# Kernel tuning notes

Measured on AMD Instinct MI355X. Metric: run time of the kernel, lower is better.

## Reference

```python
import jax, jax.numpy as jnp
import numpy as np

B, N, DIN, HID = 64, 1024, 128, 128
NEG = 9000000000000000.0


def setup_inputs() -> dict:
    key = jax.random.key(0)
    ks = jax.random.split(key, 8)
    s = 1.0 / np.sqrt(DIN)
    x = jax.random.normal(ks[0], (B, N, DIN), dtype=jnp.float32)
    mask = jax.random.randint(ks[1], (B, N, N), 0, 2, dtype=jnp.int32)
    Wv = jax.random.uniform(ks[2], (HID, DIN), jnp.float32, -s, s)
    bv = jax.random.uniform(ks[3], (HID,), jnp.float32, -s, s)
    Wk = jax.random.uniform(ks[4], (HID, DIN), jnp.float32, -s, s)
    bk = jax.random.uniform(ks[5], (HID,), jnp.float32, -s, s)
    Wq = jax.random.uniform(ks[6], (HID, DIN), jnp.float32, -s, s)
    bq = jax.random.uniform(ks[7], (HID,), jnp.float32, -s, s)
    return {"x": x, "mask": mask, "Wv": Wv, "bv": bv, "Wk": Wk, "bk": bk, "Wq": Wq, "bq": bq}


def reference(x, mask, Wv, bv, Wk, bk, Wq, bq):
    m = mask.astype(x.dtype)                       # [B,N,N]
    v = jnp.tanh(jnp.einsum('bnd,hd->bnh', x, Wv) + bv)  # [B,N,H]
    q = jnp.tanh(jnp.einsum('bnd,hd->bnh', x, Wq) + bq)
    k = jnp.tanh(jnp.einsum('bnd,hd->bnh', x, Wk) + bk)
    scores = jnp.einsum('bih,bjh->bij', q, k)      # bmm(q, k^T)
    att = jax.nn.softmax(scores * m - NEG * (1.0 - m), axis=2)
    out = jnp.einsum('bij,bjh->bih', att, v)       # [B,N,H]
    return out
```

## Files before the change

### kernel.cpp

```cpp
#include <hip/hip_runtime.h>
#include <cstdint>
#include <cstddef>

#define BB 64
#define NN 1024
#define DD 128

typedef short    bf16x8 __attribute__((ext_vector_type(8)));
typedef _Float16 f16x8  __attribute__((ext_vector_type(8)));
typedef float    f32x4  __attribute__((ext_vector_type(4)));

__device__ __forceinline__ unsigned short f2bf(float f) {
  union { float f; unsigned u; } v; v.f = f;
  unsigned r = v.u + 0x7FFFu + ((v.u >> 16) & 1u);
  return (unsigned short)(r >> 16);
}
__device__ __forceinline__ unsigned short f2h(float f) {
  union { _Float16 h; unsigned short u; } v; v.h = (_Float16)f;
  return v.u;
}
__device__ __forceinline__ float fast_tanh(float x) {
  x = fminf(15.0f, fmaxf(-15.0f, x));
  float e = __expf(2.0f * x);
  return (e - 1.0f) / (e + 1.0f);
}

__device__ __forceinline__ void async_copy16(void* lptr, const void* gptr) {
  __builtin_amdgcn_global_load_lds(
      (const __attribute__((address_space(1))) unsigned int*)gptr,
      (__attribute__((address_space(3))) unsigned int*)lptr, 16, 0, 0);
}

__global__ __launch_bounds__(256, 2) void proj_kernel(
    const float* __restrict__ x,
    const float* __restrict__ Wq, const float* __restrict__ bq,
    const float* __restrict__ Wk, const float* __restrict__ bk,
    const float* __restrict__ Wv, const float* __restrict__ bv,
    unsigned short* __restrict__ qg,
    unsigned short* __restrict__ kg,
    unsigned short* __restrict__ vtg)
{
  __shared__ unsigned short wlds[128 * 136];

  const int tid  = threadIdx.x;
  const int lane = tid & 63;
  const int wave = tid >> 6;
  const int quad = lane >> 4;
  const int mr   = lane & 15;
  const int m0   = blockIdx.x * 128;
  const int batch = m0 >> 10;
  const int n0    = m0 & 1023;

  bf16x8 xa[2][4];
#pragma unroll
  for (int mt = 0; mt < 2; ++mt) {
    const float* xr = x + (size_t)(m0 + wave * 32 + mt * 16 + mr) * DD + quad * 8;
#pragma unroll
    for (int ks = 0; ks < 4; ++ks) {
      const float4* xp = (const float4*)(xr + ks * 32);
      float4 f0 = xp[0], f1 = xp[1];
      bf16x8 f;
      f[0] = (short)f2bf(f0.x); f[1] = (short)f2bf(f0.y);
      f[2] = (short)f2bf(f0.z); f[3] = (short)f2bf(f0.w);
      f[4] = (short)f2bf(f1.x); f[5] = (short)f2bf(f1.y);
      f[6] = (short)f2bf(f1.z); f[7] = (short)f2bf(f1.w);
      xa[mt][ks] = f;
    }
  }

  const float* Wp[3] = {Wq, Wk, Wv};
  const float* bp[3] = {bq, bk, bv};

  for (int w = 0; w < 3; ++w) {
    __syncthreads();
    {
      const int row = tid >> 1, half = tid & 1;
      const float* src = Wp[w] + row * 128 + half * 64;
      unsigned short* dst = wlds + row * 136 + half * 64;
#pragma unroll
      for (int c = 0; c < 64; c += 8) {
        const float4* sp = (const float4*)(src + c);
        float4 f0 = sp[0], f1 = sp[1];
        unsigned short tmp[8];
        tmp[0] = f2bf(f0.x); tmp[1] = f2bf(f0.y); tmp[2] = f2bf(f0.z); tmp[3] = f2bf(f0.w);
        tmp[4] = f2bf(f1.x); tmp[5] = f2bf(f1.y); tmp[6] = f2bf(f1.z); tmp[7] = f2bf(f1.w);
        uint4 pk; __builtin_memcpy(&pk, tmp, 16);
        *(uint4*)(dst + c) = pk;
      }
    }
    __syncthreads();

    f32x4 z = {0.f, 0.f, 0.f, 0.f};
    f32x4 acc[2][8];
#pragma unroll
    for (int mt = 0; mt < 2; ++mt)
#pragma unroll
      for (int nt = 0; nt < 8; ++nt) acc[mt][nt] = z;

#pragma unroll
    for (int ks = 0; ks < 4; ++ks) {
#pragma unroll
      for (int nt = 0; nt < 8; ++nt) {
        bf16x8 bfr = *(const bf16x8*)(wlds + (nt * 16 + mr) * 136 + ks * 32 + quad * 8);
        acc[0][nt] = __builtin_amdgcn_mfma_f32_16x16x32_bf16(xa[0][ks], bfr, acc[0][nt], 0, 0, 0);
        acc[1][nt] = __builtin_amdgcn_mfma_f32_16x16x32_bf16(xa[1][ks], bfr, acc[1][nt], 0, 0, 0);
      }
    }

    if (w < 2) {
      unsigned short* outg = (w == 0) ? qg : kg;
#pragma unroll
      for (int mt = 0; mt < 2; ++mt) {
        const int rowbase = m0 + wave * 32 + mt * 16 + quad * 4;
#pragma unroll
        for (int nt = 0; nt < 8; ++nt) {
          float bb = bp[w][nt * 16 + mr];
#pragma unroll
          for (int r = 0; r < 4; ++r) {
            float t = fast_tanh(acc[mt][nt][r] + bb);
            outg[(size_t)(rowbase + r) * DD + nt * 16 + mr] = f2h(t);
          }
        }
      }
    } else {
      __syncthreads();
#pragma unroll
      for (int mt = 0; mt < 2; ++mt) {
        const int ib = wave * 32 + mt * 16 + quad * 4;
#pragma unroll
        for (int nt = 0; nt < 8; ++nt) {
          float bb = bp[2][nt * 16 + mr];
#pragma unroll
          for (int r = 0; r < 4; ++r) {
            float t = fast_tanh(acc[mt][nt][r] + bb);
            wlds[(nt * 16 + mr) * 136 + ib + r] = f2bf(t);
          }
        }
      }
      __syncthreads();
      const int h = tid >> 1, half = tid & 1;
      const unsigned short* src = wlds + h * 136 + half * 64;
      unsigned short* dst = vtg + (size_t)(batch * 128 + h) * NN + n0 + half * 64;
#pragma unroll
      for (int c = 0; c < 64; c += 8)
        *(uint4*)(dst + c) = *(const uint4*)(src + c);
    }
  }
}

__global__ __launch_bounds__(256, 2) void attn_kernel(
    const unsigned short* __restrict__ qg,
    const unsigned short* __restrict__ kg,
    const unsigned short* __restrict__ vtg,
    const int* __restrict__ mask,
    float* __restrict__ out)
{
  extern __shared__ unsigned short lds[];
  unsigned short* klds = lds;
  unsigned short* vlds = lds + 8192;
  unsigned short* plds = lds + 16384;

  const int tid  = threadIdx.x;
  const int lane = tid & 63;
  const int wave = tid >> 6;
  const int quad = lane >> 4;
  const int mr   = lane & 15;

  const int bx    = blockIdx.x;
  const int batch = ((bx >> 7) << 3) | (bx & 7);
  const int i0    = ((bx >> 3) & 15) * 64;

  const unsigned short* kgb = kg  + (size_t)batch * NN * DD;
  const unsigned short* vtb = vtg + (size_t)batch * DD * NN;
  const int* mrow = mask + ((size_t)batch << 20) + (size_t)(i0 + wave * 16 + mr) * NN;

  f16x8 qa[4];
#pragma unroll
  for (int ks = 0; ks < 4; ++ks)
    qa[ks] = *(const f16x8*)(qg +
        ((size_t)batch * NN + i0 + wave * 16 + mr) * DD + ks * 32 + quad * 8);

  f32x4 z = {0.f, 0.f, 0.f, 0.f};
  f32x4 o[8];
#pragma unroll
  for (int nt = 0; nt < 8; ++nt) o[nt] = z;
  float rowsum = 0.0f;

  int krow[4], kgrp[4], vrow[4], vgrp[4];
#pragma unroll
  for (int p = 0; p < 4; ++p) {
    int s = p * 256 + tid;
    krow[p] = s >> 4; kgrp[p] = (s & 15) ^ (krow[p] & 15);
    vrow[p] = s >> 3; vgrp[p] = (s & 7)  ^ (vrow[p] & 7);
  }

  int4 mreg[4];
  mreg[0] = *(const int4*)(mrow + quad * 8);
  mreg[1] = *(const int4*)(mrow + quad * 8 + 4);
  mreg[2] = *(const int4*)(mrow + 32 + quad * 8);
  mreg[3] = *(const int4*)(mrow + 32 + quad * 8 + 4);

  for (int t = 0; t < 16; ++t) {
    const int j0 = t * 64;

    unsigned mb = 0;
#pragma unroll
    for (int i = 0; i < 4; ++i) {
      mb |= (unsigned)(mreg[i].x & 1) << (i * 4 + 0);
      mb |= (unsigned)(mreg[i].y & 1) << (i * 4 + 1);
      mb |= (unsigned)(mreg[i].z & 1) << (i * 4 + 2);
      mb |= (unsigned)(mreg[i].w & 1) << (i * 4 + 3);
    }

    __syncthreads();
#pragma unroll
    for (int p = 0; p < 4; ++p) {
      int s = p * 256 + tid;
      async_copy16(klds + s * 8, kgb + (size_t)(j0 + krow[p]) * DD + kgrp[p] * 8);
    }
#pragma unroll
    for (int p = 0; p < 4; ++p) {
      int s = p * 256 + tid;
      async_copy16(vlds + s * 8, vtb + (size_t)vrow[p] * NN + j0 + vgrp[p] * 8);
    }
    __syncthreads();

    {
      const int j0n = ((t + 1) & 15) * 64;
      mreg[0] = *(const int4*)(mrow + j0n + quad * 8);
      mreg[1] = *(const int4*)(mrow + j0n + quad * 8 + 4);
      mreg[2] = *(const int4*)(mrow + j0n + 32 + quad * 8);
      mreg[3] = *(const int4*)(mrow + j0n + 32 + quad * 8 + 4);
    }

    f32x4 s[4];
#pragma unroll
    for (int nt = 0; nt < 4; ++nt) s[nt] = z;
#pragma unroll
    for (int ks = 0; ks < 4; ++ks) {
#pragma unroll
      for (int nt = 0; nt < 4; ++nt) {
        f16x8 kb = *(const f16x8*)(klds + (nt * 16 + mr) * 128 + (((ks * 4 + quad) ^ mr) * 8));
        s[nt] = __builtin_amdgcn_mfma_f32_16x16x32_f16(qa[ks], kb, s[nt], 0, 0, 0);
      }
    }

#pragma unroll
    for (int nt = 0; nt < 4; ++nt) {
#pragma unroll
      for (int r = 0; r < 4; ++r) {
        const int row = wave * 16 + quad * 4 + r;
        const int col = nt * 16 + mr;
        plds[(row << 6) + ((((col >> 3) ^ (row & 7)) << 3) | (col & 7))] =
            f2bf(__expf(s[nt][r]));
      }
    }
    __asm__ volatile("s_waitcnt lgkmcnt(0)" ::: "memory");

#pragma unroll
    for (int ks2 = 0; ks2 < 2; ++ks2) {
      bf16x8 pa = *(const bf16x8*)(plds + ((wave * 16 + mr) << 6) +
                                   ((((ks2 * 4 + quad) ^ (mr & 7)) << 3)));
      bf16x8 pm;
#pragma unroll
      for (int e = 0; e < 8; ++e) {
        unsigned bit = (mb >> (ks2 * 8 + e)) & 1u;
        short pv = bit ? pa[e] : (short)0;
        pm[e] = pv;
        union { unsigned u; float f; } cv;
        cv.u = ((unsigned)(unsigned short)pv) << 16;
        rowsum += cv.f;
      }
#pragma unroll
      for (int nt = 0; nt < 8; ++nt) {
        bf16x8 vb = *(const bf16x8*)(vlds + (nt * 16 + mr) * 64 +
                                     (((ks2 * 4 + quad) ^ (mr & 7)) * 8));
        o[nt] = __builtin_amdgcn_mfma_f32_16x16x32_bf16(pm, vb, o[nt], 0, 0, 0);
      }
    }
  }

  rowsum += __shfl_xor(rowsum, 16, 64);
  rowsum += __shfl_xor(rowsum, 32, 64);

  float* ob = out + ((size_t)batch * NN + i0) * DD;
#pragma unroll
  for (int r = 0; r < 4; ++r) {
    float rs  = __shfl(rowsum, quad * 4 + r, 64);
    float inv = 1.0f / rs;
    float* orow = ob + (size_t)(wave * 16 + quad * 4 + r) * DD + mr;
#pragma unroll
    for (int nt = 0; nt < 8; ++nt)
      orow[nt * 16] = o[nt][r] * inv;
  }
}

extern "C" void kernel_launch(void* const* d_in, const int* in_sizes, int n_in,
                              void* d_out, int out_size, void* d_ws, size_t ws_size,
                              hipStream_t stream) {
  (void)in_sizes; (void)n_in; (void)out_size; (void)ws_size;
  const float* x  = (const float*)d_in[0];
  const int* mask = (const int*)d_in[1];
  const float* Wv = (const float*)d_in[2];
  const float* bv = (const float*)d_in[3];
  const float* Wk = (const float*)d_in[4];
  const float* bk = (const float*)d_in[5];
  const float* Wq = (const float*)d_in[6];
  const float* bq = (const float*)d_in[7];
  float* out = (float*)d_out;

  unsigned short* qg  = (unsigned short*)d_ws;
  unsigned short* kg  = qg + (size_t)BB * NN * DD;
  unsigned short* vtg = kg + (size_t)BB * NN * DD;

  proj_kernel<<<512, 256, 0, stream>>>(x, Wq, bq, Wk, bk, Wv, bv, qg, kg, vtg);
  attn_kernel<<<1024, 256, 40960, stream>>>(qg, kg, vtg, mask, out);
}
```

Baseline: 481.7 us.

## Double-buffer K tiles in LDS and load V fragments directly into registers

The K tile is prefetched into an alternating LDS buffer during the current tile's QK^T MFMAs, so its async copy overlaps compute. The per-tile V staging through LDS is replaced by direct global loads of V fragments into registers, which removes one barrier per iteration. Each wave now reloads the whole V tile redundantly. The P-tile LDS swizzle is also simplified, the explicit lgkmcnt wait is dropped, and launch bounds become a waves-per-EU hint. The 64 extra VGPRs for V fragments may cut occupancy, and heavier global/L2 traffic for V is a risk.

```diff
diff --git a/kernel.cpp b/kernel.cpp
--- a/kernel.cpp
+++ b/kernel.cpp
@@ -148,7 +148,8 @@
   }
 }
 
-__global__ __launch_bounds__(256, 2) void attn_kernel(
+__attribute__((amdgpu_waves_per_eu(2, 3)))
+__global__ void attn_kernel(
     const unsigned short* __restrict__ qg,
     const unsigned short* __restrict__ kg,
     const unsigned short* __restrict__ vtg,
@@ -156,8 +157,6 @@
     float* __restrict__ out)
 {
   extern __shared__ unsigned short lds[];
-  unsigned short* klds = lds;
-  unsigned short* vlds = lds + 8192;
   unsigned short* plds = lds + 16384;
 
   const int tid  = threadIdx.x;
@@ -186,19 +185,26 @@
   for (int nt = 0; nt < 8; ++nt) o[nt] = z;
   float rowsum = 0.0f;
 
-  int krow[4], kgrp[4], vrow[4], vgrp[4];
+  int krow[4], kgrp[4];
 #pragma unroll
   for (int p = 0; p < 4; ++p) {
     int s = p * 256 + tid;
     krow[p] = s >> 4; kgrp[p] = (s & 15) ^ (krow[p] & 15);
-    vrow[p] = s >> 3; vgrp[p] = (s & 7)  ^ (vrow[p] & 7);
-  }
+  }
+
+  const int pw_swz = (wave * 4 + quad) & 7;
+  const int pr_swz = (wave * 4 + (mr >> 2)) & 7;
 
   int4 mreg[4];
   mreg[0] = *(const int4*)(mrow + quad * 8);
   mreg[1] = *(const int4*)(mrow + quad * 8 + 4);
   mreg[2] = *(const int4*)(mrow + 32 + quad * 8);
   mreg[3] = *(const int4*)(mrow + 32 + quad * 8 + 4);
+#pragma unroll
+  for (int p = 0; p < 4; ++p) {
+    int s = p * 256 + tid;
+    async_copy16(lds + s * 8, kgb + (size_t)krow[p] * DD + kgrp[p] * 8);
+  }
 
   for (int t = 0; t < 16; ++t) {
     const int j0 = t * 64;
@@ -213,17 +219,17 @@
     }
 
     __syncthreads();
-#pragma unroll
-    for (int p = 0; p < 4; ++p) {
-      int s = p * 256 + tid;
-      async_copy16(klds + s * 8, kgb + (size_t)(j0 + krow[p]) * DD + kgrp[p] * 8);
-    }
-#pragma unroll
-    for (int p = 0; p < 4; ++p) {
-      int s = p * 256 + tid;
-      async_copy16(vlds + s * 8, vtb + (size_t)vrow[p] * NN + j0 + vgrp[p] * 8);
-    }
-    __syncthreads();
+
+    unsigned short* cur = lds + ((t & 1) << 13);
+    unsigned short* nxt = lds + (((t + 1) & 1) << 13);
+
+    bf16x8 vf[2][8];
+#pragma unroll
+    for (int ks2 = 0; ks2 < 2; ++ks2)
+#pragma unroll
+      for (int nt = 0; nt < 8; ++nt)
+        vf[ks2][nt] = *(const bf16x8*)(vtb + (size_t)(nt * 16 + mr) * NN +
+                                       j0 + ks2 * 32 + quad * 8);
 
     {
       const int j0n = ((t + 1) & 15) * 64;
@@ -240,27 +246,34 @@
     for (int ks = 0; ks < 4; ++ks) {
 #pragma unroll
       for (int nt = 0; nt < 4; ++nt) {
-        f16x8 kb = *(const f16x8*)(klds + (nt * 16 + mr) * 128 + (((ks * 4 + quad) ^ mr) * 8));
+        f16x8 kb = *(const f16x8*)(cur + (nt * 16 + mr) * 128 + (((ks * 4 + quad) ^ mr) * 8));
         s[nt] = __builtin_amdgcn_mfma_f32_16x16x32_f16(qa[ks], kb, s[nt], 0, 0, 0);
       }
     }
 
+    if (t < 15) {
+      const int j0n = (t + 1) * 64;
+#pragma unroll
+      for (int p = 0; p < 4; ++p) {
+        int s2 = p * 256 + tid;
+        async_copy16(nxt + s2 * 8, kgb + (size_t)(j0n + krow[p]) * DD + kgrp[p] * 8);
+      }
+    }
+
 #pragma unroll
     for (int nt = 0; nt < 4; ++nt) {
-#pragma unroll
-      for (int r = 0; r < 4; ++r) {
-        const int row = wave * 16 + quad * 4 + r;
-        const int col = nt * 16 + mr;
-        plds[(row << 6) + ((((col >> 3) ^ (row & 7)) << 3) | (col & 7))] =
-            f2bf(__expf(s[nt][r]));
-      }
-    }
-    __asm__ volatile("s_waitcnt lgkmcnt(0)" ::: "memory");
+      const int col = nt * 16 + mr;
+      unsigned short* pbase = plds + (wave * 16 + quad * 4) * 64 +
+                              ((((col >> 3) ^ pw_swz)) << 3) + (col & 7);
+#pragma unroll
+      for (int r = 0; r < 4; ++r)
+        pbase[r * 64] = f2bf(__expf(s[nt][r]));
+    }
 
 #pragma unroll
     for (int ks2 = 0; ks2 < 2; ++ks2) {
       bf16x8 pa = *(const bf16x8*)(plds + ((wave * 16 + mr) << 6) +
-                                   ((((ks2 * 4 + quad) ^ (mr & 7)) << 3)));
+                                   (((ks2 * 4 + quad) ^ pr_swz) << 3));
       bf16x8 pm;
 #pragma unroll
       for (int e = 0; e < 8; ++e) {
@@ -272,11 +285,8 @@
         rowsum += cv.f;
       }
 #pragma unroll
-      for (int nt = 0; nt < 8; ++nt) {
-        bf16x8 vb = *(const bf16x8*)(vlds + (nt * 16 + mr) * 64 +
-                                     (((ks2 * 4 + quad) ^ (mr & 7)) * 8));
-        o[nt] = __builtin_amdgcn_mfma_f32_16x16x32_bf16(pm, vb, o[nt], 0, 0, 0);
-      }
+      for (int nt = 0; nt < 8; ++nt)
+        o[nt] = __builtin_amdgcn_mfma_f32_16x16x32_bf16(pm, vf[ks2][nt], o[nt], 0, 0, 0);
     }
   }
 
```

Result: slower. 539.7 us (+12.0%).
